# Kernel tuning notes

Measured on AMD Instinct MI355X. Metric: run time of the kernel, lower is better.

The kernel has to match this reference:

```python
import jax, jax.numpy as jnp
import numpy as np

B, S, D = 4, 1024, 512
H, HD, M = 8, 64, 2
EPS = 1e-5


def setup_inputs() -> dict:
    key = jax.random.key(0)
    ks = jax.random.split(key, 8)
    scale = 0.02
    x = jax.random.normal(ks[0], (B, S, D), dtype=jnp.float32)
    Wq = jax.random.normal(ks[1], (D, D), dtype=jnp.float32) * scale
    Wk = jax.random.normal(ks[2], (D, D), dtype=jnp.float32) * scale
    Wv = jax.random.normal(ks[3], (D, D), dtype=jnp.float32) * scale
    Wo = jax.random.normal(ks[4], (D, D), dtype=jnp.float32) * scale
    bo = jnp.zeros((D,), dtype=jnp.float32)
    Wg = jax.random.normal(ks[5], (H * (2 + M), D), dtype=jnp.float32) * scale
    bg = jnp.zeros((H * (2 + M),), dtype=jnp.float32)
    init_decays = jnp.array([0.95, 0.8], dtype=jnp.float32)
    logit = jnp.log(init_decays / (1.0 - init_decays))
    logit_alphas = jnp.tile(logit[None, :], (H, 1))  # [H, M]
    ln_w = jnp.ones((D,), dtype=jnp.float32)
    ln_b = jnp.zeros((D,), dtype=jnp.float32)
    return {"x": x, "Wq": Wq, "Wk": Wk, "Wv": Wv, "Wo": Wo, "bo": bo,
            "Wg": Wg, "bg": bg, "logit_alphas": logit_alphas,
            "ln_w": ln_w, "ln_b": ln_b}


def _rope(x):
    # x: [B, S, H, HD] interleaved rotary
    half = HD // 2
    inv_freq = 1.0 / (10000.0 ** (jnp.arange(half, dtype=jnp.float32) / half))
    t = jnp.arange(S, dtype=jnp.float32)
    freqs = t[:, None] * inv_freq[None, :]            # [S, half]
    cos = jnp.cos(freqs)[None, :, None, :]            # [1, S, 1, half]
    sin = jnp.sin(freqs)[None, :, None, :]
    x1, x2 = x[..., ::2], x[..., 1::2]
    o1 = x1 * cos - x2 * sin
    o2 = x1 * sin + x2 * cos
    return jnp.stack((o1, o2), axis=-1).reshape(x.shape)


def _forward(x, Wq, Wk, Wv, Wo, bo, Wg, bg, logit_alphas, ln_w, ln_b):
    residual = x
    q = (x @ Wq.T).reshape(B, S, H, HD)
    k = (x @ Wk.T).reshape(B, S, H, HD)
    v = (x @ Wv.T).reshape(B, S, H, HD)
    q = _rope(q)
    k = _rope(k)

    gates = (x @ Wg.T + bg).reshape(B, S, H, 2 + M)
    g_f = jax.nn.sigmoid(gates[..., 0])               # [B, S, H]
    g_u = jax.nn.sigmoid(gates[..., 1])               # [B, S, H]
    w_mix = jax.nn.softmax(gates[..., 2:], axis=-1)   # [B, S, H, M]
    alphas = jax.nn.sigmoid(logit_alphas)             # [H, M]

    # time-major for scan
    qs = jnp.moveaxis(q, 1, 0)       # [S, B, H, HD]
    ks = jnp.moveaxis(k, 1, 0)
    vs = jnp.moveaxis(v, 1, 0)
    gfs = jnp.moveaxis(g_f, 1, 0)    # [S, B, H]
    gus = jnp.moveaxis(g_u, 1, 0)
    wms = jnp.moveaxis(w_mix, 1, 0)  # [S, B, H, M]

    state0 = jnp.zeros((B, H, M, HD, HD), dtype=x.dtype)

    def step(state, inp):
        qt, kt, vt, gf, gu, wt = inp
        retain = alphas[None, :, :] * gf[:, :, None]           # [B, H, M]
        write_w = wt * gu[..., None]                           # [B, H, M]
        outer = jnp.einsum('bhd,bhe->bhde', kt, vt)            # [B, H, HD, HD]
        state = (state * retain[..., None, None]
                 + outer[:, :, None, :, :] * write_w[..., None, None])
        S_read = jnp.einsum('bhmde,bhm->bhde', state, wt)      # [B, H, HD, HD]
        o = jnp.einsum('bhd,bhde->bhe', qt, S_read)            # [B, H, HD]
        return state, o

    _, outs = jax.lax.scan(step, state0, (qs, ks, vs, gfs, gus, wms))
    out = jnp.moveaxis(outs, 0, 1).reshape(B, S, H * HD)
    out = out @ Wo.T + bo
    y = residual + out
    mu = jnp.mean(y, axis=-1, keepdims=True)
    var = jnp.mean(jnp.square(y - mu), axis=-1, keepdims=True)
    return (y - mu) / jnp.sqrt(var + EPS) * ln_w + ln_b


def reference(x, Wq, Wk, Wv, Wo, bo, Wg, bg, logit_alphas, ln_w, ln_b):
    return _forward(x, Wq, Wk, Wv, Wo, bo, Wg, bg, logit_alphas, ln_w, ln_b)
```

## Files before the change

### kernel.cpp

```cpp
#include <hip/hip_runtime.h>
#include <hip/hip_bf16.h>
#include <math.h>

#define B_  4
#define S_  1024
#define D_  512
#define H_  8
#define HD_ 64
#define EPS_ 1e-5f

typedef __attribute__((ext_vector_type(8))) short  bf16x8;
typedef __attribute__((ext_vector_type(4))) float  f32x4;

#define MFMA16(a, b, c) __builtin_amdgcn_mfma_f32_16x16x32_bf16((a), (b), (c), 0, 0, 0)

#define GLOAD16(gp, lp) __builtin_amdgcn_global_load_lds( \
    (const __attribute__((address_space(1))) unsigned int*)(gp), \
    (__attribute__((address_space(3))) unsigned int*)(lp), 16, 0, 0)

__device__ __forceinline__ float bf2f(short u) {
    union { unsigned int i; float f; } v;
    v.i = ((unsigned int)(unsigned short)u) << 16;
    return v.f;
}
__device__ __forceinline__ short f2bf(float f) {
    __hip_bfloat16 h = __float2bfloat16(f);
    return *reinterpret_cast<short*>(&h);
}

__global__ __launch_bounds__(256) void convert_inputs(
    const float* __restrict__ x,
    const float* __restrict__ Wq, const float* __restrict__ Wk,
    const float* __restrict__ Wv, const float* __restrict__ Wg,
    const float* __restrict__ Wo,
    short* __restrict__ xbf, short* __restrict__ Wcat, short* __restrict__ Wobf,
    float2* __restrict__ rope)
{
    const int id = blockIdx.x * 256 + threadIdx.x;
    if (id < 262144) {
        const size_t e = (size_t)id * 8;
        float4 v0 = *(const float4*)(x + e);
        float4 v1 = *(const float4*)(x + e + 4);
        bf16x8 o = { f2bf(v0.x), f2bf(v0.y), f2bf(v0.z), f2bf(v0.w),
                     f2bf(v1.x), f2bf(v1.y), f2bf(v1.z), f2bf(v1.w) };
        *(bf16x8*)(xbf + e) = o;
    } else if (id < 368640) {
        const int i2 = id - 262144;
        const int row = i2 >> 6;
        const int c8 = (i2 & 63) * 8;
        const float* s = nullptr;
        if (row < 512)       s = Wq + (size_t)row * 512 + c8;
        else if (row < 1024) s = Wk + (size_t)(row - 512) * 512 + c8;
        else if (row < 1536) s = Wv + (size_t)(row - 1024) * 512 + c8;
        else if (row < 1568) s = Wg + (size_t)(row - 1536) * 512 + c8;
        bf16x8 o = (bf16x8)0;
        if (s) {
            float4 v0 = *(const float4*)(s);
            float4 v1 = *(const float4*)(s + 4);
            o = bf16x8{ f2bf(v0.x), f2bf(v0.y), f2bf(v0.z), f2bf(v0.w),
                        f2bf(v1.x), f2bf(v1.y), f2bf(v1.z), f2bf(v1.w) };
        }
        *(bf16x8*)(Wcat + (size_t)row * 512 + c8) = o;
    } else if (id < 401408) {
        const int i3 = id - 368640;
        const size_t e = (size_t)i3 * 8;
        float4 v0 = *(const float4*)(Wo + e);
        float4 v1 = *(const float4*)(Wo + e + 4);
        bf16x8 o = { f2bf(v0.x), f2bf(v0.y), f2bf(v0.z), f2bf(v0.w),
                     f2bf(v1.x), f2bf(v1.y), f2bf(v1.z), f2bf(v1.w) };
        *(bf16x8*)(Wobf + e) = o;
    } else {
        const int i4 = id - 401408;
        const int s = i4 >> 5, i = i4 & 31;
        const float inv = exp2f(-(float)i * (13.287712379549449f / 32.0f));
        float sn, cs;
        sincosf((float)s * inv, &sn, &cs);
        rope[i4] = make_float2(cs, sn);
    }
}

__global__ __launch_bounds__(256) void proj_scan_a(
    const short* __restrict__ xbf, const short* __restrict__ Wcat,
    const float2* __restrict__ rope, const float* __restrict__ bg,
    const float* __restrict__ logit_alphas,
    short* __restrict__ Qbf, short* __restrict__ Kbf, short* __restrict__ Vbf,
    short* __restrict__ Ubuf, float* __restrict__ SRb, float* __restrict__ SCAL)
{
    __shared__ __align__(16) char smem[58368];
    short* sQ   = (short*)(smem);
    short* sK   = (short*)(smem + 9216);
    short* sVT  = (short*)(smem + 18432);
    short* sP   = (short*)(smem + 27648);
    short* sSTb = (short*)(smem + 36864);
    float (*sScal)[6] = (float(*)[6])(smem + 55296);
    float* sKs  = (float*)(smem + 56832);
    float* sG   = (float*)(smem + 57344);
    short* Bstage = sQ;
    short* Astage = sSTb;

    const int tid = threadIdx.x;
    const int wave = tid >> 6, lane = tid & 63;
    const int lrow = lane & 15, lgrp = lane >> 4;
    const int c  = blockIdx.x & 15;
    const int bh = blockIdx.x >> 4;
    const int h = bh & 7, b = bh >> 3;
    const int s0 = c * 64;
    const int row0 = wave * 16;
    const int srl = lane >> 3;
    const int scs = (lane & 7) * 8;

    f32x4 acc[13];
    #pragma unroll
    for (int n = 0; n < 13; ++n) acc[n] = (f32x4)0.f;

    for (int step = 0; step < 8; ++step) {
        const int kt = step * 64;
        #pragma unroll
        for (int i = 0; i < 2; ++i) {
            const int ch = wave * 2 + i;
            const size_t gr = (size_t)(b * S_ + s0 + ch * 8 + srl) * 512 + kt + scs;
            GLOAD16(xbf + gr, Astage + ch * 512);
        }
        #pragma unroll
        for (int i = 0; i < 7; ++i) {
            const int ch = i * 4 + wave;
            if (ch < 26) {
                int grow;
                if (ch < 8)       grow = h * 64 + ch * 8;
                else if (ch < 16) grow = 512 + h * 64 + (ch - 8) * 8;
                else if (ch < 24) grow = 1024 + h * 64 + (ch - 16) * 8;
                else              grow = 1536 + h * 4 + (ch - 24) * 8;
                GLOAD16(Wcat + (size_t)(grow + srl) * 512 + kt + scs, Bstage + ch * 512);
            }
        }
        __syncthreads();
        #pragma unroll
        for (int kk = 0; kk < 2; ++kk) {
            const int kb = kk * 32 + lgrp * 8;
            bf16x8 a = *(const bf16x8*)&Astage[(row0 + lrow) * 64 + kb];
            #pragma unroll
            for (int n = 0; n < 13; ++n) {
                bf16x8 bb = *(const bf16x8*)&Bstage[(n * 16 + lrow) * 64 + kb];
                acc[n] = MFMA16(a, bb, acc[n]);
            }
        }
        __syncthreads();
    }

    #pragma unroll
    for (int n = 0; n < 4; ++n)
        #pragma unroll
        for (int j = 0; j < 4; ++j) {
            const int r = row0 + lgrp * 4 + j;
            sQ[r * 72 + n * 16 + lrow]    = f2bf(acc[n][j]);
            sK[r * 72 + n * 16 + lrow]    = f2bf(acc[4 + n][j]);
            const short vb = f2bf(acc[8 + n][j]);
            sVT[(n * 16 + lrow) * 72 + r] = vb;
            sP [r * 72 + n * 16 + lrow]   = vb;
        }
    if (lrow < 4)
        #pragma unroll
        for (int j = 0; j < 4; ++j)
            sG[(row0 + lgrp * 4 + j) * 4 + lrow] = acc[12][j];
    __syncthreads();

    if (tid < 64) {
        const float g0 = sG[tid * 4 + 0] + bg[h * 4 + 0];
        const float g1 = sG[tid * 4 + 1] + bg[h * 4 + 1];
        const float g2 = sG[tid * 4 + 2] + bg[h * 4 + 2];
        const float g3 = sG[tid * 4 + 3] + bg[h * 4 + 3];
        const float gf  = 1.f / (1.f + expf(-g0));
        const float gu  = 1.f / (1.f + expf(-g1));
        const float wm0 = 1.f / (1.f + expf(-(g2 - g3)));
        const float a0 = 1.f / (1.f + expf(-logit_alphas[h * 2 + 0]));
        const float a1 = 1.f / (1.f + expf(-logit_alphas[h * 2 + 1]));
        sScal[tid][0] = a0 * gf; sScal[tid][1] = a1 * gf;
        sScal[tid][2] = wm0 * gu; sScal[tid][3] = (1.f - wm0) * gu;
        sScal[tid][4] = wm0; sScal[tid][5] = 1.f - wm0;
    }
    #pragma unroll
    for (int it = 0; it < 2; ++it) {
        const int i = tid + it * 256;
        const int r = i >> 3, c8 = (i & 7) * 8;
        const int s = s0 + r;
        bf16x8 q8 = *(const bf16x8*)&sQ[r * 72 + c8];
        bf16x8 k8 = *(const bf16x8*)&sK[r * 72 + c8];
        bf16x8 qo, ko;
        #pragma unroll
        for (int j = 0; j < 4; ++j) {
            const float2 t = rope[s * 32 + (c8 >> 1) + j];
            const float qx = bf2f(q8[2 * j]), qy = bf2f(q8[2 * j + 1]);
            const float kx = bf2f(k8[2 * j]), ky = bf2f(k8[2 * j + 1]);
            qo[2 * j]     = f2bf(qx * t.x - qy * t.y);
            qo[2 * j + 1] = f2bf(qx * t.y + qy * t.x);
            ko[2 * j]     = f2bf(kx * t.x - ky * t.y);
            ko[2 * j + 1] = f2bf(kx * t.y + ky * t.x);
        }
        *(bf16x8*)&sQ[r * 72 + c8] = qo;
        *(bf16x8*)&sK[r * 72 + c8] = ko;
    }
    #pragma unroll
    for (int it = 0; it < 2; ++it) {
        const int i = tid + it * 256;
        const int r = i >> 3, seg = (i & 7) * 8;
        *(bf16x8*)(Vbf + ((size_t)(b * S_ + s0 + r)) * 512 + h * 64 + seg) =
            *(const bf16x8*)&sP[r * 72 + seg];
    }
    __syncthreads();

    if (wave < 2) {
        const int m = wave;
        float pre = log2f(sScal[lane][m]);
        #pragma unroll
        for (int off = 1; off < 64; off <<= 1) {
            const float u = __shfl_up(pre, off);
            if (lane >= off) pre += u;
        }
        const float lR = __shfl(pre, 63);
        sKs[m * 64 + lane] = sScal[lane][2 + m] * exp2f(lR - pre);
        float* sc = SCAL + ((size_t)(bh * S_) + s0 + lane) * 8;
        sc[0 + m] = pre;
        sc[2 + m] = sScal[lane][2 + m];
        sc[4 + m] = sScal[lane][4 + m];
        sc[6 + m] = sScal[lane][4 + m] * exp2f(pre);
        if (lane == 63) SRb[blockIdx.x * 2 + m] = exp2f(lR);
    }
    #pragma unroll
    for (int it = 0; it < 2; ++it) {
        const int i = tid + it * 256;
        const int r = i >> 3, seg = (i & 7) * 8;
        const size_t g = ((size_t)(b * S_ + s0 + r)) * 512 + h * 64 + seg;
        *(bf16x8*)(Qbf + g) = *(const bf16x8*)&sQ[r * 72 + seg];
        *(bf16x8*)(Kbf + g) = *(const bf16x8*)&sK[r * 72 + seg];
    }
    __syncthreads();

    {
        const int task = tid >> 1, halfd = tid & 1;
        const int m = task >> 6, tau = task & 63;
        short* kt_ = sSTb + m * 4608;
        const float ksc = sKs[m * 64 + tau];
        #pragma unroll
        for (int dd = halfd * 32; dd < halfd * 32 + 32; dd += 8) {
            bf16x8 kr = *(const bf16x8*)&sK[tau * 72 + dd];
            #pragma unroll
            for (int j = 0; j < 8; ++j)
                kt_[(dd + j) * 72 + tau] = f2bf(bf2f(kr[j]) * ksc);
        }
    }
    __syncthreads();

    #pragma unroll
    for (int m = 0; m < 2; ++m) {
        f32x4 accU[4];
        #pragma unroll
        for (int db = 0; db < 4; ++db) accU[db] = (f32x4)0.f;
        const short* kt_ = sSTb + m * 4608;
        #pragma unroll
        for (int kk = 0; kk < 2; ++kk) {
            const int kb = kk * 32 + lgrp * 8;
            bf16x8 a = *(const bf16x8*)&sVT[(row0 + lrow) * 72 + kb];
            #pragma unroll
            for (int db = 0; db < 4; ++db) {
                bf16x8 bb = *(const bf16x8*)&kt_[(db * 16 + lrow) * 72 + kb];
                accU[db] = MFMA16(a, bb, accU[db]);
            }
        }
        __syncthreads();
        #pragma unroll
        for (int db = 0; db < 4; ++db)
            #pragma unroll
            for (int r = 0; r < 4; ++r) {
                const int e = row0 + lgrp * 4 + r;
                sP[e * 72 + db * 16 + lrow] = f2bf(accU[db][r]);
            }
        __syncthreads();
        short* ub = Ubuf + ((size_t)blockIdx.x * 2 + m) * 4096;
        #pragma unroll
        for (int it = 0; it < 2; ++it) {
            const int i = tid + it * 256;
            const int e = i >> 3, seg = (i & 7) * 8;
            *(bf16x8*)(ub + e * 64 + seg) = *(const bf16x8*)&sP[e * 72 + seg];
        }
    }
}

__global__ __launch_bounds__(256) void chunk_o(
    const short* __restrict__ Qbf, const short* __restrict__ Kbf,
    const short* __restrict__ Vbf, const float* __restrict__ SCAL,
    const short* __restrict__ Ubuf, const float* __restrict__ SRb,
    short* __restrict__ Obf)
{
    __shared__ __align__(16) short sQ [64 * 72];
    __shared__ __align__(16) short sK [64 * 72];
    __shared__ __align__(16) short sVT[64 * 72];
    __shared__ __align__(16) short sP [64 * 72];
    __shared__ __align__(16) short sST[2][64 * 72];
    __shared__ float sScal[64][8];

    const int tid  = threadIdx.x;
    const int wave = tid >> 6, lane = tid & 63;
    const int lrow = lane & 15, lgrp = lane >> 4;
    const int c  = blockIdx.x & 15;
    const int bh = blockIdx.x >> 4;
    const int h = bh & 7, b = bh >> 3;
    const int row0 = wave * 16;
    const int s0 = c * 64;

    if (tid < 64) {
        const float* sc = SCAL + ((size_t)(bh * S_) + s0 + tid) * 8;
        *(float4*)&sScal[tid][0] = *(const float4*)sc;
        *(float4*)&sScal[tid][4] = *(const float4*)(sc + 4);
    }

    float sp[4][8];
    #pragma unroll
    for (int g = 0; g < 4; ++g)
        #pragma unroll
        for (int j = 0; j < 8; ++j) sp[g][j] = 0.f;
    for (int cp = 0; cp < c; ++cp) {
        const int bhc = bh * 16 + cp;
        const float R0 = SRb[bhc * 2 + 0];
        const float R1 = SRb[bhc * 2 + 1];
        const short* ub = Ubuf + (size_t)bhc * 8192;
        #pragma unroll
        for (int g = 0; g < 4; ++g) {
            bf16x8 u = *(const bf16x8*)(ub + g * 2048 + tid * 8);
            const float R = (g < 2) ? R0 : R1;
            #pragma unroll
            for (int j = 0; j < 8; ++j) sp[g][j] = fmaf(R, sp[g][j], bf2f(u[j]));
        }
    }
    #pragma unroll
    for (int g = 0; g < 4; ++g) {
        const int i = g * 2048 + tid * 8;
        const int m = i >> 12, e = (i >> 6) & 63, d = i & 63;
        bf16x8 o;
        #pragma unroll
        for (int j = 0; j < 8; ++j) o[j] = f2bf(sp[g][j]);
        *(bf16x8*)&sST[m][e * 72 + d] = o;
    }

    #pragma unroll
    for (int it = 0; it < 2; ++it) {
        const int i = tid + it * 256;
        const int r = i >> 3, c8 = (i & 7) * 8;
        const size_t g = ((size_t)(b * S_ + s0 + r)) * 512 + h * 64 + c8;
        *(bf16x8*)&sQ[r * 72 + c8] = *(const bf16x8*)(Qbf + g);
        *(bf16x8*)&sK[r * 72 + c8] = *(const bf16x8*)(Kbf + g);
        bf16x8 v8 = *(const bf16x8*)(Vbf + g);
        #pragma unroll
        for (int j = 0; j < 8; ++j) sVT[(c8 + j) * 72 + r] = v8[j];
    }
    __syncthreads();

    f32x4 accS[4], accO[4];
    #pragma unroll
    for (int cb = 0; cb < 4; ++cb) { accS[cb] = (f32x4)0.f; accO[cb] = (f32x4)0.f; }
    #pragma unroll
    for (int kk = 0; kk < 2; ++kk) {
        const int kb = kk * 32 + lgrp * 8;
        bf16x8 a = *(const bf16x8*)&sQ[(row0 + lrow) * 72 + kb];
        #pragma unroll
        for (int cb = 0; cb < 4; ++cb) {
            bf16x8 bb = *(const bf16x8*)&sK[(cb * 16 + lrow) * 72 + kb];
            accS[cb] = MFMA16(a, bb, accS[cb]);
        }
    }

    #pragma unroll
    for (int kk = 0; kk < 4; ++kk) {
        const int k0 = kk * 32 + lgrp * 8;
        const int m = k0 >> 6, d0 = k0 & 63;
        const float qs = sScal[row0 + lrow][6 + m];
        bf16x8 qr = *(const bf16x8*)&sQ[(row0 + lrow) * 72 + d0];
        bf16x8 a;
        #pragma unroll
        for (int j = 0; j < 8; ++j) a[j] = f2bf(bf2f(qr[j]) * qs);
        #pragma unroll
        for (int cb = 0; cb < 4; ++cb) {
            bf16x8 bb = *(const bf16x8*)&sST[m][(cb * 16 + lrow) * 72 + d0];
            accO[cb] = MFMA16(a, bb, accO[cb]);
        }
    }

    #pragma unroll
    for (int r = 0; r < 4; ++r) {
        const int t = row0 + lgrp * 4 + r;
        const float wm0 = sScal[t][4], wm1 = sScal[t][5];
        const float lc0t = sScal[t][0], lc1t = sScal[t][1];
        #pragma unroll
        for (int cb = 0; cb < 4; ++cb) {
            const int tau = cb * 16 + lrow;
            float p = 0.f;
            if (tau <= t) {
                const float c0 = wm0 * sScal[tau][2] * exp2f(lc0t - sScal[tau][0]);
                const float c1 = wm1 * sScal[tau][3] * exp2f(lc1t - sScal[tau][1]);
                p = accS[cb][r] * (c0 + c1);
            }
            sP[t * 72 + tau] = f2bf(p);
        }
    }

    #pragma unroll
    for (int kk = 0; kk < 2; ++kk) {
        const int kb = kk * 32 + lgrp * 8;
        bf16x8 a = *(const bf16x8*)&sP[(row0 + lrow) * 72 + kb];
        #pragma unroll
        for (int cb = 0; cb < 4; ++cb) {
            bf16x8 bb = *(const bf16x8*)&sVT[(cb * 16 + lrow) * 72 + kb];
            accO[cb] = MFMA16(a, bb, accO[cb]);
        }
    }

    #pragma unroll
    for (int cb = 0; cb < 4; ++cb)
        #pragma unroll
        for (int r = 0; r < 4; ++r) {
            const int t = row0 + lgrp * 4 + r;
            sP[t * 72 + cb * 16 + lrow] = f2bf(accO[cb][r]);
        }
    __syncthreads();
    #pragma unroll
    for (int it = 0; it < 2; ++it) {
        const int i = tid + it * 256;
        const int t = i >> 3, seg = (i & 7) * 8;
        *(bf16x8*)(Obf + ((size_t)(b * S_ + s0 + t)) * 512 + h * 64 + seg) =
            *(const bf16x8*)&sP[t * 72 + seg];
    }
}

__global__ __launch_bounds__(256) void mfma_out(
    const short* __restrict__ Abf, const short* __restrict__ Wobf,
    const float* __restrict__ bo, const float* __restrict__ xres,
    short* __restrict__ Ybf)
{
    __shared__ __align__(16) short lds[24576];

    const int p = blockIdx.x;
    const int xcd = p & 7, slot = p >> 3;
    const int by = xcd + 8 * (slot >> 3);
    const int bx = slot & 7;
    const int n0 = bx * 64, m0 = by * 128;

    const int tid = threadIdx.x;
    const int lane = tid & 63, wave = tid >> 6;
    const int lrow = lane & 15, lgrp = lane >> 4;
    const int wr = wave >> 1, wc = wave & 1;
    const int srl = lane >> 3;
    const int scs = (lane & 7) * 8;

    f32x4 acc[4][2];
    #pragma unroll
    for (int i = 0; i < 4; ++i)
        #pragma unroll
        for (int j = 0; j < 2; ++j) acc[i][j] = (f32x4)0.f;

    #define OUT_STAGE(buf, kt)  {                                             \
        short* dA = lds + (buf) * 12288;                                      \
        short* dB = dA + 8192;                                                \
        _Pragma("unroll")                                                     \
        for (int i = 0; i < 4; ++i) {                                         \
            const int chunk = i * 4 + wave;                                   \
            const int r = chunk * 8 + srl;                                    \
            GLOAD16(Abf + (size_t)(m0 + r) * 512 + (kt) + scs, dA + chunk * 512); \
        }                                                                     \
        _Pragma("unroll")                                                     \
        for (int i = 0; i < 2; ++i) {                                         \
            const int chunk = i * 4 + wave;                                   \
            const int r = chunk * 8 + srl;                                    \
            GLOAD16(Wobf + (size_t)(n0 + r) * 512 + (kt) + scs, dB + chunk * 512); \
        } }

    OUT_STAGE(0, 0);
    __syncthreads();
    int cur = 0;
    for (int step = 0; step < 8; ++step) {
        if (step < 7) OUT_STAGE(cur ^ 1, (step + 1) * 64);
        const short* sA = lds + cur * 12288;
        const short* sB = sA + 8192;
        #pragma unroll
        for (int kk = 0; kk < 2; ++kk) {
            const int kb = kk * 32 + lgrp * 8;
            bf16x8 af[4], bfr[2];
            #pragma unroll
            for (int mi = 0; mi < 4; ++mi)
                af[mi] = *(const bf16x8*)&sA[(wr * 64 + mi * 16 + lrow) * 64 + kb];
            #pragma unroll
            for (int ni = 0; ni < 2; ++ni)
                bfr[ni] = *(const bf16x8*)&sB[(wc * 32 + ni * 16 + lrow) * 64 + kb];
            #pragma unroll
            for (int mi = 0; mi < 4; ++mi)
                #pragma unroll
                for (int ni = 0; ni < 2; ++ni)
                    acc[mi][ni] = MFMA16(af[mi], bfr[ni], acc[mi][ni]);
        }
        __syncthreads();
        cur ^= 1;
    }
    #undef OUT_STAGE

    short* stg = lds;
    #pragma unroll
    for (int mi = 0; mi < 4; ++mi)
        #pragma unroll
        for (int ni = 0; ni < 2; ++ni)
            #pragma unroll
            for (int j = 0; j < 4; ++j) {
                const int rl = wr * 64 + mi * 16 + lgrp * 4 + j;
                const int cl = wc * 32 + ni * 16 + lrow;
                stg[rl * 80 + cl] = f2bf(acc[mi][ni][j]);
            }
    __syncthreads();
    #pragma unroll
    for (int it = 0; it < 4; ++it) {
        const int u = tid + it * 256;
        const int row = u >> 3, seg = (u & 7) * 8;
        const size_t gbase = (size_t)(m0 + row) * 512 + n0 + seg;
        bf16x8 a = *(const bf16x8*)&stg[row * 80 + seg];
        float4 x0 = *(const float4*)(xres + gbase);
        float4 x1 = *(const float4*)(xres + gbase + 4);
        float4 b0 = *(const float4*)(bo + n0 + seg);
        float4 b1 = *(const float4*)(bo + n0 + seg + 4);
        bf16x8 y;
        y[0] = f2bf(bf2f(a[0]) + b0.x + x0.x);
        y[1] = f2bf(bf2f(a[1]) + b0.y + x0.y);
        y[2] = f2bf(bf2f(a[2]) + b0.z + x0.z);
        y[3] = f2bf(bf2f(a[3]) + b0.w + x0.w);
        y[4] = f2bf(bf2f(a[4]) + b1.x + x1.x);
        y[5] = f2bf(bf2f(a[5]) + b1.y + x1.y);
        y[6] = f2bf(bf2f(a[6]) + b1.z + x1.z);
        y[7] = f2bf(bf2f(a[7]) + b1.w + x1.w);
        *(bf16x8*)(Ybf + gbase) = y;
    }
}

__global__ __launch_bounds__(256) void ln_kernel(
    const short* __restrict__ Ybf, const float* __restrict__ ln_w,
    const float* __restrict__ ln_b, float* __restrict__ out)
{
    const int wave = threadIdx.x >> 6;
    const int lane = threadIdx.x & 63;
    const int row = blockIdx.x * 4 + wave;

    bf16x8 v8 = *(const bf16x8*)(Ybf + (size_t)row * 512 + lane * 8);
    float v[8];
    #pragma unroll
    for (int j = 0; j < 8; ++j) v[j] = bf2f(v8[j]);

    float s = 0.f, sq = 0.f;
    #pragma unroll
    for (int j = 0; j < 8; ++j) { s += v[j]; sq += v[j] * v[j]; }
    #pragma unroll
    for (int off = 32; off; off >>= 1) {
        s  += __shfl_xor(s,  off);
        sq += __shfl_xor(sq, off);
    }
    const float mu  = s * (1.f / 512.f);
    const float var = sq * (1.f / 512.f) - mu * mu;
    const float inv = rsqrtf(var + EPS_);

    float4 w0 = *(const float4*)(ln_w + lane * 8);
    float4 w1 = *(const float4*)(ln_w + lane * 8 + 4);
    float4 b0 = *(const float4*)(ln_b + lane * 8);
    float4 b1 = *(const float4*)(ln_b + lane * 8 + 4);
    float4 o0, o1;
    o0.x = (v[0] - mu) * inv * w0.x + b0.x;
    o0.y = (v[1] - mu) * inv * w0.y + b0.y;
    o0.z = (v[2] - mu) * inv * w0.z + b0.z;
    o0.w = (v[3] - mu) * inv * w0.w + b0.w;
    o1.x = (v[4] - mu) * inv * w1.x + b1.x;
    o1.y = (v[5] - mu) * inv * w1.y + b1.y;
    o1.z = (v[6] - mu) * inv * w1.z + b1.z;
    o1.w = (v[7] - mu) * inv * w1.w + b1.w;
    *(float4*)(out + (size_t)row * 512 + lane * 8)     = o0;
    *(float4*)(out + (size_t)row * 512 + lane * 8 + 4) = o1;
}

extern "C" void kernel_launch(void* const* d_in, const int* in_sizes, int n_in,
                              void* d_out, int out_size, void* d_ws, size_t ws_size,
                              hipStream_t stream)
{
    const float* x   = (const float*)d_in[0];
    const float* Wq  = (const float*)d_in[1];
    const float* Wk  = (const float*)d_in[2];
    const float* Wv  = (const float*)d_in[3];
    const float* Wo  = (const float*)d_in[4];
    const float* bo  = (const float*)d_in[5];
    const float* Wg  = (const float*)d_in[6];
    const float* bg  = (const float*)d_in[7];
    const float* la  = (const float*)d_in[8];
    const float* lnw = (const float*)d_in[9];
    const float* lnb = (const float*)d_in[10];

    const size_t NQ = (size_t)B_ * S_ * D_;
    float* ROPE = (float*)d_ws;
    float* SRb  = ROPE + 65536;
    float* SCAL = SRb + 1024;
    short* xbf  = (short*)(SCAL + 262144);
    short* Wcat = xbf + NQ;
    short* Wobf = Wcat + (size_t)1664 * 512;
    short* Qbf  = Wobf + (size_t)512 * 512;
    short* Kbf  = Qbf + NQ;
    short* Vbf  = Kbf + NQ;
    short* Obf  = Vbf + NQ;
    short* Ybf  = Obf + NQ;
    short* Ubuf = Ybf + NQ;

    convert_inputs<<<1696, 256, 0, stream>>>(x, Wq, Wk, Wv, Wg, Wo, xbf, Wcat, Wobf,
                                             (float2*)ROPE);
    proj_scan_a<<<512, 256, 0, stream>>>(xbf, Wcat, (const float2*)ROPE, bg, la,
                                         Qbf, Kbf, Vbf, Ubuf, SRb, SCAL);
    chunk_o<<<512, 256, 0, stream>>>(Qbf, Kbf, Vbf, SCAL, Ubuf, SRb, Obf);
    mfma_out<<<256, 256, 0, stream>>>(Obf, Wobf, bo, x, Ybf);
    ln_kernel<<<1024, 256, 0, stream>>>(Ybf, lnw, lnb, (float*)d_out);
}
```

Before: 132.7 us.

## Fuse output projection with residual and LayerNorm into one full-row kernel

Replaces the tiled output-projection GEMM and the separate LayerNorm kernel with one kernel in which each 512-thread block computes 16 complete rows across all 512 output columns. Bias, residual and LayerNorm are then applied in fp32 from LDS, so the bf16 Y intermediate and one kernel launch go away. In exchange the GEMM loses double-buffered prefetch and reloads the entire Wo tile for every 16-row block, which raises L2 traffic and exposes load latency at each k-step.

```diff
diff --git a/kernel.cpp b/kernel.cpp
--- a/kernel.cpp
+++ b/kernel.cpp
@@ -430,151 +430,100 @@
     }
 }
 
-__global__ __launch_bounds__(256) void mfma_out(
+__global__ __launch_bounds__(512) void mfma_out_ln(
     const short* __restrict__ Abf, const short* __restrict__ Wobf,
     const float* __restrict__ bo, const float* __restrict__ xres,
-    short* __restrict__ Ybf)
+    const float* __restrict__ ln_w, const float* __restrict__ ln_b,
+    float* __restrict__ out)
 {
-    __shared__ __align__(16) short lds[24576];
-
-    const int p = blockIdx.x;
-    const int xcd = p & 7, slot = p >> 3;
-    const int by = xcd + 8 * (slot >> 3);
-    const int bx = slot & 7;
-    const int n0 = bx * 64, m0 = by * 128;
-
+    __shared__ __align__(16) short lds[33792];
+    short* sA = lds;
+    short* sB = lds + 1024;
+    float* yf = (float*)lds;
+
+    const int m0 = blockIdx.x * 16;
     const int tid = threadIdx.x;
-    const int lane = tid & 63, wave = tid >> 6;
+    const int wave = tid >> 6, lane = tid & 63;
     const int lrow = lane & 15, lgrp = lane >> 4;
-    const int wr = wave >> 1, wc = wave & 1;
     const int srl = lane >> 3;
     const int scs = (lane & 7) * 8;
 
-    f32x4 acc[4][2];
-    #pragma unroll
-    for (int i = 0; i < 4; ++i)
-        #pragma unroll
-        for (int j = 0; j < 2; ++j) acc[i][j] = (f32x4)0.f;
-
-    #define OUT_STAGE(buf, kt)  {                                             \
-        short* dA = lds + (buf) * 12288;                                      \
-        short* dB = dA + 8192;                                                \
-        _Pragma("unroll")                                                     \
-        for (int i = 0; i < 4; ++i) {                                         \
-            const int chunk = i * 4 + wave;                                   \
-            const int r = chunk * 8 + srl;                                    \
-            GLOAD16(Abf + (size_t)(m0 + r) * 512 + (kt) + scs, dA + chunk * 512); \
-        }                                                                     \
-        _Pragma("unroll")                                                     \
-        for (int i = 0; i < 2; ++i) {                                         \
-            const int chunk = i * 4 + wave;                                   \
-            const int r = chunk * 8 + srl;                                    \
-            GLOAD16(Wobf + (size_t)(n0 + r) * 512 + (kt) + scs, dB + chunk * 512); \
-        } }
-
-    OUT_STAGE(0, 0);
-    __syncthreads();
-    int cur = 0;
+    f32x4 acc[4];
+    #pragma unroll
+    for (int cb = 0; cb < 4; ++cb) acc[cb] = (f32x4)0.f;
+
     for (int step = 0; step < 8; ++step) {
-        if (step < 7) OUT_STAGE(cur ^ 1, (step + 1) * 64);
-        const short* sA = lds + cur * 12288;
-        const short* sB = sA + 8192;
+        const int kt = step * 64;
+        if (wave < 2)
+            GLOAD16(Abf + (size_t)(m0 + wave * 8 + srl) * 512 + kt + scs,
+                    sA + wave * 512);
+        #pragma unroll
+        for (int i = 0; i < 8; ++i) {
+            const int ch = wave * 8 + i;
+            GLOAD16(Wobf + (size_t)(ch * 8 + srl) * 512 + kt + scs,
+                    sB + ch * 512);
+        }
+        __syncthreads();
         #pragma unroll
         for (int kk = 0; kk < 2; ++kk) {
             const int kb = kk * 32 + lgrp * 8;
-            bf16x8 af[4], bfr[2];
+            bf16x8 a = *(const bf16x8*)&sA[lrow * 64 + kb];
             #pragma unroll
-            for (int mi = 0; mi < 4; ++mi)
-                af[mi] = *(const bf16x8*)&sA[(wr * 64 + mi * 16 + lrow) * 64 + kb];
-            #pragma unroll
-            for (int ni = 0; ni < 2; ++ni)
-                bfr[ni] = *(const bf16x8*)&sB[(wc * 32 + ni * 16 + lrow) * 64 + kb];
-            #pragma unroll
-            for (int mi = 0; mi < 4; ++mi)
-                #pragma unroll
-                for (int ni = 0; ni < 2; ++ni)
-                    acc[mi][ni] = MFMA16(af[mi], bfr[ni], acc[mi][ni]);
+            for (int cb = 0; cb < 4; ++cb) {
+                bf16x8 bb = *(const bf16x8*)&sB[(wave * 64 + cb * 16 + lrow) * 64 + kb];
+                acc[cb] = MFMA16(a, bb, acc[cb]);
+            }
         }
         __syncthreads();
-        cur ^= 1;
-    }
-    #undef OUT_STAGE
-
-    short* stg = lds;
-    #pragma unroll
-    for (int mi = 0; mi < 4; ++mi)
-        #pragma unroll
-        for (int ni = 0; ni < 2; ++ni)
-            #pragma unroll
-            for (int j = 0; j < 4; ++j) {
-                const int rl = wr * 64 + mi * 16 + lgrp * 4 + j;
-                const int cl = wc * 32 + ni * 16 + lrow;
-                stg[rl * 80 + cl] = f2bf(acc[mi][ni][j]);
-            }
-    __syncthreads();
-    #pragma unroll
-    for (int it = 0; it < 4; ++it) {
-        const int u = tid + it * 256;
-        const int row = u >> 3, seg = (u & 7) * 8;
-        const size_t gbase = (size_t)(m0 + row) * 512 + n0 + seg;
-        bf16x8 a = *(const bf16x8*)&stg[row * 80 + seg];
-        float4 x0 = *(const float4*)(xres + gbase);
-        float4 x1 = *(const float4*)(xres + gbase + 4);
-        float4 b0 = *(const float4*)(bo + n0 + seg);
-        float4 b1 = *(const float4*)(bo + n0 + seg + 4);
-        bf16x8 y;
-        y[0] = f2bf(bf2f(a[0]) + b0.x + x0.x);
-        y[1] = f2bf(bf2f(a[1]) + b0.y + x0.y);
-        y[2] = f2bf(bf2f(a[2]) + b0.z + x0.z);
-        y[3] = f2bf(bf2f(a[3]) + b0.w + x0.w);
-        y[4] = f2bf(bf2f(a[4]) + b1.x + x1.x);
-        y[5] = f2bf(bf2f(a[5]) + b1.y + x1.y);
-        y[6] = f2bf(bf2f(a[6]) + b1.z + x1.z);
-        y[7] = f2bf(bf2f(a[7]) + b1.w + x1.w);
-        *(bf16x8*)(Ybf + gbase) = y;
-    }
-}
-
-__global__ __launch_bounds__(256) void ln_kernel(
-    const short* __restrict__ Ybf, const float* __restrict__ ln_w,
-    const float* __restrict__ ln_b, float* __restrict__ out)
-{
-    const int wave = threadIdx.x >> 6;
-    const int lane = threadIdx.x & 63;
-    const int row = blockIdx.x * 4 + wave;
-
-    bf16x8 v8 = *(const bf16x8*)(Ybf + (size_t)row * 512 + lane * 8);
-    float v[8];
-    #pragma unroll
-    for (int j = 0; j < 8; ++j) v[j] = bf2f(v8[j]);
-
-    float s = 0.f, sq = 0.f;
-    #pragma unroll
-    for (int j = 0; j < 8; ++j) { s += v[j]; sq += v[j] * v[j]; }
-    #pragma unroll
-    for (int off = 32; off; off >>= 1) {
-        s  += __shfl_xor(s,  off);
-        sq += __shfl_xor(sq, off);
-    }
-    const float mu  = s * (1.f / 512.f);
-    const float var = sq * (1.f / 512.f) - mu * mu;
-    const float inv = rsqrtf(var + EPS_);
-
-    float4 w0 = *(const float4*)(ln_w + lane * 8);
-    float4 w1 = *(const float4*)(ln_w + lane * 8 + 4);
-    float4 b0 = *(const float4*)(ln_b + lane * 8);
-    float4 b1 = *(const float4*)(ln_b + lane * 8 + 4);
-    float4 o0, o1;
-    o0.x = (v[0] - mu) * inv * w0.x + b0.x;
-    o0.y = (v[1] - mu) * inv * w0.y + b0.y;
-    o0.z = (v[2] - mu) * inv * w0.z + b0.z;
-    o0.w = (v[3] - mu) * inv * w0.w + b0.w;
-    o1.x = (v[4] - mu) * inv * w1.x + b1.x;
-    o1.y = (v[5] - mu) * inv * w1.y + b1.y;
-    o1.z = (v[6] - mu) * inv * w1.z + b1.z;
-    o1.w = (v[7] - mu) * inv * w1.w + b1.w;
-    *(float4*)(out + (size_t)row * 512 + lane * 8)     = o0;
-    *(float4*)(out + (size_t)row * 512 + lane * 8 + 4) = o1;
+    }
+
+    #pragma unroll
+    for (int cb = 0; cb < 4; ++cb) {
+        const int col = wave * 64 + cb * 16 + lrow;
+        const float bb = bo[col];
+        #pragma unroll
+        for (int j = 0; j < 4; ++j)
+            yf[(lgrp * 4 + j) * 520 + col] = acc[cb][j] + bb;
+    }
+    __syncthreads();
+
+    #pragma unroll
+    for (int rr = 0; rr < 2; ++rr) {
+        const int r = wave * 2 + rr;
+        const int grow = m0 + r;
+        float4 y0 = *(const float4*)&yf[r * 520 + lane * 8];
+        float4 y1 = *(const float4*)&yf[r * 520 + lane * 8 + 4];
+        const float4 x0 = *(const float4*)(xres + (size_t)grow * 512 + lane * 8);
+        const float4 x1 = *(const float4*)(xres + (size_t)grow * 512 + lane * 8 + 4);
+        y0.x += x0.x; y0.y += x0.y; y0.z += x0.z; y0.w += x0.w;
+        y1.x += x1.x; y1.y += x1.y; y1.z += x1.z; y1.w += x1.w;
+        float s  = y0.x + y0.y + y0.z + y0.w + y1.x + y1.y + y1.z + y1.w;
+        float sq = y0.x*y0.x + y0.y*y0.y + y0.z*y0.z + y0.w*y0.w
+                 + y1.x*y1.x + y1.y*y1.y + y1.z*y1.z + y1.w*y1.w;
+        #pragma unroll
+        for (int off = 32; off; off >>= 1) {
+            s  += __shfl_xor(s,  off);
+            sq += __shfl_xor(sq, off);
+        }
+        const float mu  = s * (1.f / 512.f);
+        const float var = sq * (1.f / 512.f) - mu * mu;
+        const float inv = rsqrtf(var + EPS_);
+        const float4 w0 = *(const float4*)(ln_w + lane * 8);
+        const float4 w1 = *(const float4*)(ln_w + lane * 8 + 4);
+        const float4 b0 = *(const float4*)(ln_b + lane * 8);
+        const float4 b1 = *(const float4*)(ln_b + lane * 8 + 4);
+        float4 o0, o1;
+        o0.x = (y0.x - mu) * inv * w0.x + b0.x;
+        o0.y = (y0.y - mu) * inv * w0.y + b0.y;
+        o0.z = (y0.z - mu) * inv * w0.z + b0.z;
+        o0.w = (y0.w - mu) * inv * w0.w + b0.w;
+        o1.x = (y1.x - mu) * inv * w1.x + b1.x;
+        o1.y = (y1.y - mu) * inv * w1.y + b1.y;
+        o1.z = (y1.z - mu) * inv * w1.z + b1.z;
+        o1.w = (y1.w - mu) * inv * w1.w + b1.w;
+        *(float4*)(out + (size_t)grow * 512 + lane * 8)     = o0;
+        *(float4*)(out + (size_t)grow * 512 + lane * 8 + 4) = o1;
+    }
 }
 
 extern "C" void kernel_launch(void* const* d_in, const int* in_sizes, int n_in,
@@ -604,14 +553,12 @@
     short* Kbf  = Qbf + NQ;
     short* Vbf  = Kbf + NQ;
     short* Obf  = Vbf + NQ;
-    short* Ybf  = Obf + NQ;
-    short* Ubuf = Ybf + NQ;
+    short* Ubuf = Obf + NQ;
 
     convert_inputs<<<1696, 256, 0, stream>>>(x, Wq, Wk, Wv, Wg, Wo, xbf, Wcat, Wobf,
                                              (float2*)ROPE);
     proj_scan_a<<<512, 256, 0, stream>>>(xbf, Wcat, (const float2*)ROPE, bg, la,
                                          Qbf, Kbf, Vbf, Ubuf, SRb, SCAL);
     chunk_o<<<512, 256, 0, stream>>>(Qbf, Kbf, Vbf, SCAL, Ubuf, SRb, Obf);
-    mfma_out<<<256, 256, 0, stream>>>(Obf, Wobf, bo, x, Ybf);
-    ln_kernel<<<1024, 256, 0, stream>>>(Ybf, lnw, lnb, (float*)d_out);
-}
+    mfma_out_ln<<<256, 512, 0, stream>>>(Obf, Wobf, bo, x, lnw, lnb, (float*)d_out);
+}
```

Measured after the change: 138.6 us. 4.5% more time.
